# Optimization experiments

Measured on AMD Instinct MI355X. Metric: run time of the kernel, lower is better.

The kernel has to match this reference:

```python
import jax, jax.numpy as jnp
import numpy as np

TOP_K = 2  # num_experts_per_tok


def setup_inputs() -> dict:
    key = jax.random.key(0)
    ks = jax.random.split(key, 5)
    B, S, D, M, E = 4, 2048, 2048, 2048, 8
    x = jax.random.normal(ks[0], (B, S, D), dtype=jnp.float32)
    gate_kernel = jax.random.normal(ks[1], (D, E), dtype=jnp.float32) / np.sqrt(D)
    wi_0 = jax.random.normal(ks[2], (E, D, M), dtype=jnp.float32) / np.sqrt(D)
    wi_1 = jax.random.normal(ks[3], (E, D, M), dtype=jnp.float32) / np.sqrt(D)
    wo = jax.random.normal(ks[4], (E, M, D), dtype=jnp.float32) / np.sqrt(M)
    return {"x": x, "gate_kernel": gate_kernel, "wi_0": wi_0, "wi_1": wi_1, "wo": wo}


def reference(x, gate_kernel, wi_0, wi_1, wo):
    E = gate_kernel.shape[-1]
    # Gate logits: (B, S, E)
    gate_logits = jnp.einsum("bsd,de->bse", x, gate_kernel)
    # Top-k routing, then softmax over the selected experts' logits
    top_k_weights, top_k_indices = jax.lax.top_k(gate_logits, TOP_K)
    top_k_weights = jax.nn.softmax(top_k_weights.astype(jnp.float32), axis=-1).astype(x.dtype)
    # Dense combine weights per expert: (B, S, E)
    combine_w = jnp.sum(
        jax.nn.one_hot(top_k_indices, E, dtype=x.dtype) * top_k_weights[..., None], axis=-2
    )
    # Grouped GEMM (dense-masked form, as in MaxText dense_matmul path)
    h0 = jnp.einsum("bsd,edm->bsem", x, wi_0)  # (B, S, E, M)
    h1 = jnp.einsum("bsd,edm->bsem", x, wi_1)
    h = jax.nn.silu(h0) * h1 * combine_w[..., None]
    out = jnp.einsum("bsem,emd->bsd", h, wo)  # (B, S, D)
    return out
```

## Files before the change

### kernel.cpp

```cpp
#include <hip/hip_runtime.h>
#include <hip/hip_bf16.h>
#include <stdint.h>

#define TT   8192
#define DD   2048
#define MM   2048
#define NE   8

typedef float f32x4 __attribute__((ext_vector_type(4)));
typedef short s16x8 __attribute__((ext_vector_type(8)));
typedef unsigned int u32;
typedef unsigned long long u64;

static __device__ __forceinline__ short f2bf(float f) {
  __hip_bfloat16 h = __float2bfloat16(f);
  short s;
  __builtin_memcpy(&s, &h, 2);
  return s;
}
static __device__ __forceinline__ float bf2f(short s) {
  u32 u = ((u32)(unsigned short)s) << 16;
  float f;
  __builtin_memcpy(&f, &u, 4);
  return f;
}

static __device__ __forceinline__ void gload_lds16(const short* g, short* lds) {
  __builtin_amdgcn_global_load_lds(
      (const __attribute__((address_space(1))) u32*)g,
      (__attribute__((address_space(3))) u32*)lds, 16, 0, 0);
}

#define VM2()  asm volatile("s_waitcnt vmcnt(2)" ::: "memory")
#define VM0()  asm volatile("s_waitcnt vmcnt(0)" ::: "memory")
#define LG0()  asm volatile("s_waitcnt lgkmcnt(0)" ::: "memory")
#define BAR()  __builtin_amdgcn_s_barrier()

__global__ __launch_bounds__(256) void tcvt01_kernel(
    const float* __restrict__ w0, const float* __restrict__ w1,
    short* __restrict__ o0, short* __restrict__ o1) {
  __shared__ short tile[64][65];
  const int bz = blockIdx.z;
  const float* in  = (bz < 8) ? w0 : w1;
  short* out       = (bz < 8) ? o0 : o1;
  const int ex = bz & 7;
  const float* src = in + (size_t)ex * DD * MM;
  short* dst = out + (size_t)ex * DD * MM;
  const int r0 = blockIdx.y * 64;
  const int c0 = blockIdx.x * 64;
  const int t = threadIdx.x;
  const int rr = t >> 4, cc = (t & 15) * 4;
  #pragma unroll
  for (int i = 0; i < 4; i++) {
    int row = rr + i * 16;
    f32x4 v = *(const f32x4*)(src + (size_t)(r0 + row) * MM + c0 + cc);
    tile[cc + 0][row] = f2bf(v[0]);
    tile[cc + 1][row] = f2bf(v[1]);
    tile[cc + 2][row] = f2bf(v[2]);
    tile[cc + 3][row] = f2bf(v[3]);
  }
  __syncthreads();
  const int orow = t >> 2, c8 = (t & 3) * 16;
  s16x8 v0, v1;
  #pragma unroll
  for (int i = 0; i < 8; i++) { v0[i] = tile[orow][c8 + i]; v1[i] = tile[orow][c8 + 8 + i]; }
  short* dp = dst + (size_t)(c0 + orow) * DD + r0 + c8;
  *(s16x8*)(dp) = v0;
  *(s16x8*)(dp + 8) = v1;
}

__global__ __launch_bounds__(256) void gate_kernel(const float* __restrict__ x,
    const float* __restrict__ gk, int* __restrict__ counts,
    int* __restrict__ tkidx, float* __restrict__ tkw, short* __restrict__ xbf) {
  int t = blockIdx.x;
  const float* xr = x + (size_t)t * DD;
  const int d0 = threadIdx.x * 8;
  f32x4 a = *(const f32x4*)(xr + d0);
  f32x4 b = *(const f32x4*)(xr + d0 + 4);
  s16x8 v;
  v[0]=f2bf(a[0]); v[1]=f2bf(a[1]); v[2]=f2bf(a[2]); v[3]=f2bf(a[3]);
  v[4]=f2bf(b[0]); v[5]=f2bf(b[1]); v[6]=f2bf(b[2]); v[7]=f2bf(b[3]);
  *(s16x8*)(xbf + (size_t)t * DD + d0) = v;

  float acc[NE];
  #pragma unroll
  for (int e = 0; e < NE; e++) acc[e] = 0.f;
  #pragma unroll
  for (int j = 0; j < 8; j++) {
    float xv = (j < 4) ? a[j] : b[j - 4];
    const float* g = gk + (size_t)(d0 + j) * NE;
    #pragma unroll
    for (int e = 0; e < NE; e++) acc[e] += xv * g[e];
  }
  #pragma unroll
  for (int e = 0; e < NE; e++) {
    #pragma unroll
    for (int off = 32; off >= 1; off >>= 1)
      acc[e] += __shfl_xor(acc[e], off, 64);
  }
  __shared__ float red[4][NE];
  int wid = threadIdx.x >> 6;
  int lane = threadIdx.x & 63;
  if (lane == 0) {
    #pragma unroll
    for (int e = 0; e < NE; e++) red[wid][e] = acc[e];
  }
  __syncthreads();
  if (threadIdx.x == 0) {
    float l[NE];
    #pragma unroll
    for (int e = 0; e < NE; e++) l[e] = red[0][e] + red[1][e] + red[2][e] + red[3][e];
    int i1 = 0; float v1 = l[0];
    #pragma unroll
    for (int e = 1; e < NE; e++) if (l[e] > v1) { v1 = l[e]; i1 = e; }
    int i2 = -1; float v2 = -1e30f;
    #pragma unroll
    for (int e = 0; e < NE; e++) if (e != i1 && l[e] > v2) { v2 = l[e]; i2 = e; }
    float p = __expf(v2 - v1);
    float inv = 1.f / (1.f + p);
    tkidx[t*2]   = i1; tkidx[t*2+1] = i2;
    tkw[t*2]     = inv; tkw[t*2+1]  = p * inv;
    atomicAdd(&counts[i1], 1);
    atomicAdd(&counts[i2], 1);
  }
}

__global__ __launch_bounds__(256) void scatter_kernel(const int* __restrict__ counts,
    int* __restrict__ offsets, const int* __restrict__ tkidx,
    const float* __restrict__ tkw, int* __restrict__ ltok, float* __restrict__ lwt,
    int* __restrict__ slots) {
  const int e = blockIdx.x;
  const int tid = threadIdx.x;
  const int wid = tid >> 6, lane = tid & 63;
  __shared__ int base_s;
  __shared__ int wsum[4];
  if (tid == 0) {
    int s = 0;
    #pragma unroll
    for (int i = 0; i < NE; i++) {
      if (e == 0) offsets[i] = s;
      if (i < e) s += counts[i];
      else if (e == 0) s += counts[i];
    }
    if (e == 0) offsets[NE] = s;
    int bs = 0;
    for (int i = 0; i < e; i++) bs += counts[i];
    base_s = bs;
  }
  __syncthreads();
  int base = base_s;
  for (int it = 0; it < (TT * 2) / 256; it++) {
    int i = it * 256 + tid;
    bool m = (tkidx[i] == e);
    u64 b = __ballot(m);
    if (lane == 0) wsum[wid] = __popcll(b);
    __syncthreads();
    int pre = 0;
    #pragma unroll
    for (int w = 0; w < 4; w++) if (w < wid) pre += wsum[w];
    int tot = wsum[0] + wsum[1] + wsum[2] + wsum[3];
    int rank = __popcll(b & ((lane == 0) ? 0ull : ((1ull << lane) - 1ull)));
    if (m) {
      int dst = base + pre + rank;
      ltok[dst] = i >> 1;
      lwt[dst]  = tkw[i];
      slots[i]  = dst;
    }
    __syncthreads();
    base += tot;
  }
}

__global__ __launch_bounds__(256) void combine_kernel(const short* __restrict__ comb,
    const int* __restrict__ slots, float* __restrict__ out) {
  const int t = blockIdx.x;
  const int s0 = slots[2 * t], s1 = slots[2 * t + 1];
  const int idx = threadIdx.x;
  s16x8 a = *(const s16x8*)(comb + (size_t)s0 * DD + idx * 8);
  s16x8 b = *(const s16x8*)(comb + (size_t)s1 * DD + idx * 8);
  f32x4 o0, o1;
  #pragma unroll
  for (int j = 0; j < 4; j++) {
    o0[j] = bf2f(a[j]) + bf2f(b[j]);
    o1[j] = bf2f(a[4 + j]) + bf2f(b[4 + j]);
  }
  float* po = out + (size_t)t * DD + idx * 8;
  *(f32x4*)(po) = o0;
  *(f32x4*)(po + 4) = o1;
}

__device__ __forceinline__ void find_seg(const int* __restrict__ offsets, int tile, int bm,
                                         int& e, int& row0, int& rows, int& seg) {
  e = -1; row0 = 0; rows = 0; seg = 0;
  int accT = 0, prev = offsets[0];
  #pragma unroll
  for (int i = 0; i < NE; i++) {
    int nxt = offsets[i+1];
    int cnt = nxt - prev;
    int nt = (cnt + bm - 1) / bm;
    if (e < 0 && tile < accT + nt) { e = i; row0 = (tile - accT) * bm; rows = cnt; seg = prev; }
    accT += nt; prev = nxt;
  }
}

__device__ __forceinline__ void xcd_map(int ypx, int& tile, int& nyi) {
  const int bid = blockIdx.y * gridDim.x + blockIdx.x;
  const int xcd = bid & 7;
  const int i = bid >> 3;
  tile = i / ypx;
  nyi  = xcd * ypx + (i % ypx);
}

#define G1TILES 136
#define G1GRID  (G1TILES * 16)
#define GOGRID  (8 * 32 * 32)

__global__ __launch_bounds__(256, 2) void gemm1_fused(
    const short* __restrict__ xbf,
    const short* __restrict__ w0t, const short* __restrict__ w1t,
    const int* __restrict__ offsets,
    const int* __restrict__ ltok, const float* __restrict__ lwt,
    short* __restrict__ hbuf,
    const float* __restrict__ wo, short* __restrict__ wot) {
  __shared__ short As[128 * 64];
  __shared__ short B0s[128 * 64];
  __shared__ short B1s[128 * 64];
  __shared__ float w_s[128];

  const int bid = blockIdx.x;
  if (bid >= G1GRID) {
    short (*tile)[65] = (short(*)[65])As;
    const int idx = bid - G1GRID;
    const int ex = idx >> 10;
    const int rem = idx & 1023;
    const int r0 = (rem >> 5) * 64;
    const int c0 = (rem & 31) * 64;
    const float* src = wo + (size_t)ex * DD * MM;
    short* dst = wot + (size_t)ex * DD * MM;
    const int t = threadIdx.x;
    const int rr = t >> 4, cc = (t & 15) * 4;
    #pragma unroll
    for (int i = 0; i < 4; i++) {
      int row = rr + i * 16;
      f32x4 v = *(const f32x4*)(src + (size_t)(r0 + row) * MM + c0 + cc);
      tile[cc + 0][row] = f2bf(v[0]);
      tile[cc + 1][row] = f2bf(v[1]);
      tile[cc + 2][row] = f2bf(v[2]);
      tile[cc + 3][row] = f2bf(v[3]);
    }
    __syncthreads();
    const int orow = t >> 2, c8 = (t & 3) * 16;
    s16x8 v0, v1;
    #pragma unroll
    for (int i = 0; i < 8; i++) { v0[i] = tile[orow][c8 + i]; v1[i] = tile[orow][c8 + 8 + i]; }
    short* dp = dst + (size_t)(c0 + orow) * DD + r0 + c8;
    *(s16x8*)(dp) = v0;
    *(s16x8*)(dp + 8) = v1;
    return;
  }

  const int xcd = bid & 7;
  const int bi = bid >> 3;
  const int tile = bi >> 1;
  const int nyi = xcd * 2 + (bi & 1);
  const int n0 = nyi * 128;
  int e, row0, rows, seg;
  find_seg(offsets, tile, 128, e, row0, rows, seg);
  if (e < 0) return;

  const int tid = threadIdx.x;
  const int lane = tid & 63, wid = tid >> 6;
  if (tid < 128) {
    int gr = row0 + tid;
    w_s[tid] = (gr < rows) ? lwt[seg + gr] : 0.f;
  }

  const int swz = ((lane & 7) ^ (lane >> 3)) * 8;
  const short* abase[4];
  const short* b0base[4];
  const short* b1base[4];
  #pragma unroll
  for (int c = 0; c < 4; c++) {
    int chunk = wid * 4 + c;
    int r = chunk * 8 + (lane >> 3);
    int gr = row0 + r; if (gr >= rows) gr = rows - 1;
    int tok = ltok[seg + gr];
    abase[c]  = xbf + (size_t)tok * DD + swz;
    int n = n0 + r;
    b0base[c] = w0t + ((size_t)e * MM + n) * DD + swz;
    b1base[c] = w1t + ((size_t)e * MM + n) * DD + swz;
  }

  const int wr = wid >> 1, wc = wid & 1;
  const int lr = lane & 15;
  const int kq = (lane >> 4) * 8;

  f32x4 acc0[4][4], acc1[4][4];
  #pragma unroll
  for (int i = 0; i < 4; i++)
    #pragma unroll
    for (int j = 0; j < 4; j++) { acc0[i][j] = 0.f; acc1[i][j] = 0.f; }

  for (int k0 = 0; k0 < DD; k0 += 64) {
    #pragma unroll
    for (int c = 0; c < 4; c++) {
      int chunk = wid * 4 + c;
      gload_lds16(abase[c]  + k0, As  + chunk * 512);
      gload_lds16(b0base[c] + k0, B0s + chunk * 512);
      gload_lds16(b1base[c] + k0, B1s + chunk * 512);
    }
    __syncthreads();

    #pragma unroll
    for (int ks = 0; ks < 2; ks++) {
      s16x8 a[4], b0[4], b1[4];
      #pragma unroll
      for (int mi = 0; mi < 4; mi++) {
        int row = wr * 64 + mi * 16 + lr;
        int koff = (ks * 32 + kq) ^ ((row & 7) * 8);
        a[mi] = *(const s16x8*)&As[row * 64 + koff];
      }
      #pragma unroll
      for (int ni = 0; ni < 4; ni++) {
        int row = wc * 64 + ni * 16 + lr;
        int koff = (ks * 32 + kq) ^ ((row & 7) * 8);
        b0[ni] = *(const s16x8*)&B0s[row * 64 + koff];
        b1[ni] = *(const s16x8*)&B1s[row * 64 + koff];
      }
      #pragma unroll
      for (int mi = 0; mi < 4; mi++)
        #pragma unroll
        for (int ni = 0; ni < 4; ni++) {
          acc0[mi][ni] = __builtin_amdgcn_mfma_f32_16x16x32_bf16(a[mi], b0[ni], acc0[mi][ni], 0, 0, 0);
          acc1[mi][ni] = __builtin_amdgcn_mfma_f32_16x16x32_bf16(a[mi], b1[ni], acc1[mi][ni], 0, 0, 0);
        }
    }
    __syncthreads();
  }

  const int lq = lane >> 4;
  #pragma unroll
  for (int mi = 0; mi < 4; mi++) {
    #pragma unroll
    for (int jj = 0; jj < 4; jj++) {
      int r = wr * 64 + mi * 16 + lq * 4 + jj;
      int gr = row0 + r;
      if (gr < rows) {
        float wgt = w_s[r];
        size_t hrow = (size_t)(seg + gr) * MM + n0;
        #pragma unroll
        for (int ni = 0; ni < 4; ni++) {
          int c = wc * 64 + ni * 16 + lr;
          float g = acc0[mi][ni][jj];
          float u = acc1[mi][ni][jj];
          float act = g / (1.f + __expf(-g));
          hbuf[hrow + c] = f2bf(act * u * wgt);
        }
      }
    }
  }
}

#define MAXT2 72

__global__ __launch_bounds__(512, 2) void gemm2_fast(
    const short* __restrict__ hbuf,
    const short* __restrict__ wot,
    const int* __restrict__ offsets,
    short* __restrict__ comb) {
  __shared__ short As[2][256 * 64];
  __shared__ short Bs[2][256 * 64];

  int tile, nyi;
  xcd_map(1, tile, nyi);
  const int n0 = nyi * 256;
  int e, row0, rows, seg;
  find_seg(offsets, tile, 256, e, row0, rows, seg);
  if (e < 0) return;

  const int tid = threadIdx.x;
  const int lane = tid & 63, wid = tid >> 6;
  const int srow = tid >> 3;
  const int swz = ((tid & 7) ^ (srow & 7)) * 8;

  const short* aP[2][2];
  const short* bP[2][2];
  #pragma unroll
  for (int h = 0; h < 2; h++)
    #pragma unroll
    for (int rd = 0; rd < 2; rd++) {
      int gr = row0 + h * 128 + rd * 64 + srow;
      if (gr >= rows) gr = rows - 1;
      aP[h][rd] = hbuf + (size_t)(seg + gr) * MM + swz;
      int n = n0 + h * 128 + rd * 64 + srow;
      bP[h][rd] = wot + ((size_t)e * DD + n) * MM + swz;
    }
  const short* aP00 = aP[0][0]; const short* aP01 = aP[0][1];
  const short* aP10 = aP[1][0]; const short* aP11 = aP[1][1];
  const short* bP00 = bP[0][0]; const short* bP01 = bP[0][1];
  const short* bP10 = bP[1][0]; const short* bP11 = bP[1][1];

  const int wr = wid >> 2, wn = wid & 3;
  const int lr = lane & 15;
  const int kq = (lane >> 4) * 8;
  const int lq = lane >> 4;

  f32x4 acc[8][4];
  #pragma unroll
  for (int i = 0; i < 8; i++)
    #pragma unroll
    for (int j = 0; j < 4; j++) acc[i][j] = 0.f;

  int brow_[4], bkey_[4];
  #pragma unroll
  for (int ni = 0; ni < 4; ni++) {
    brow_[ni] = wn * 64 + ni * 16 + lr;
    bkey_[ni] = (brow_[ni] & 7) * 8;
  }
  int arowL_[4], akeyL_[4], arowH_[4], akeyH_[4];
  #pragma unroll
  for (int mi = 0; mi < 4; mi++) {
    arowL_[mi] = wr * 128 + mi * 16 + lr;        akeyL_[mi] = (arowL_[mi] & 7) * 8;
    arowH_[mi] = wr * 128 + (mi + 4) * 16 + lr;  akeyH_[mi] = (arowH_[mi] & 7) * 8;
  }

  const int wofs = wid * 512;
  auto stA0 = [&](int buf, int kof) {
    short* d = &As[buf][0];
    gload_lds16(aP00 + kof, d + wofs);
    gload_lds16(aP01 + kof, d + 4096 + wofs);
  };
  auto stA1 = [&](int buf, int kof) {
    short* d = &As[buf][128 * 64];
    gload_lds16(aP10 + kof, d + wofs);
    gload_lds16(aP11 + kof, d + 4096 + wofs);
  };
  auto stB0 = [&](int buf, int kof) {
    short* d = &Bs[buf][0];
    gload_lds16(bP00 + kof, d + wofs);
    gload_lds16(bP01 + kof, d + 4096 + wofs);
  };
  auto stB1 = [&](int buf, int kof) {
    short* d = &Bs[buf][128 * 64];
    gload_lds16(bP10 + kof, d + wofs);
    gload_lds16(bP11 + kof, d + 4096 + wofs);
  };

  stA0(0, 0); stB0(0, 0); stB1(0, 0); stA1(0, 0);
  stA0(1, 64);
  VM2();
  BAR();

  const int NIT = (MM / 64) / 2;
  s16x8 av[4], bv[4], bw[4];

  for (int it = 0; it < NIT; ++it) {
    const bool pf = (it + 1 < NIT);
    const int kb  = (2 * it + 1) * 64;
    const int kna = (2 * it + 2) * 64;
    const int knb = (2 * it + 3) * 64;

    #pragma unroll
    for (int mi = 0; mi < 4; mi++) av[mi] = *(const s16x8*)&As[0][arowL_[mi] * 64 + (kq ^ akeyL_[mi])];
    #pragma unroll
    for (int ni = 0; ni < 4; ni++) bv[ni] = *(const s16x8*)&Bs[0][brow_[ni] * 64 + (kq ^ bkey_[ni])];
    stB0(1, kb);
    BAR(); LG0();
    __builtin_amdgcn_s_setprio(1);
    #pragma unroll
    for (int mi = 0; mi < 4; mi++)
      #pragma unroll
      for (int ni = 0; ni < 4; ni++)
        acc[mi][ni] = __builtin_amdgcn_mfma_f32_16x16x32_bf16(av[mi], bv[ni], acc[mi][ni], 0, 0, 0);
    __builtin_amdgcn_s_setprio(0);
    BAR();

    #pragma unroll
    for (int mi = 0; mi < 4; mi++) av[mi] = *(const s16x8*)&As[0][arowH_[mi] * 64 + (kq ^ akeyH_[mi])];
    stB1(1, kb);
    BAR(); LG0();
    __builtin_amdgcn_s_setprio(1);
    #pragma unroll
    for (int mi = 0; mi < 4; mi++)
      #pragma unroll
      for (int ni = 0; ni < 4; ni++)
        acc[mi + 4][ni] = __builtin_amdgcn_mfma_f32_16x16x32_bf16(av[mi], bv[ni], acc[mi + 4][ni], 0, 0, 0);
    __builtin_amdgcn_s_setprio(0);
    BAR();

    #pragma unroll
    for (int mi = 0; mi < 4; mi++) av[mi] = *(const s16x8*)&As[0][arowL_[mi] * 64 + ((32 + kq) ^ akeyL_[mi])];
    #pragma unroll
    for (int ni = 0; ni < 4; ni++) bw[ni] = *(const s16x8*)&Bs[0][brow_[ni] * 64 + ((32 + kq) ^ bkey_[ni])];
    stA1(1, kb);
    BAR(); LG0();
    __builtin_amdgcn_s_setprio(1);
    #pragma unroll
    for (int mi = 0; mi < 4; mi++)
      #pragma unroll
      for (int ni = 0; ni < 4; ni++)
        acc[mi][ni] = __builtin_amdgcn_mfma_f32_16x16x32_bf16(av[mi], bw[ni], acc[mi][ni], 0, 0, 0);
    __builtin_amdgcn_s_setprio(0);
    BAR();

    #pragma unroll
    for (int mi = 0; mi < 4; mi++) av[mi] = *(const s16x8*)&As[0][arowH_[mi] * 64 + ((32 + kq) ^ akeyH_[mi])];
    if (pf) stA0(0, kna);
    BAR(); LG0();
    __builtin_amdgcn_s_setprio(1);
    #pragma unroll
    for (int mi = 0; mi < 4; mi++)
      #pragma unroll
      for (int ni = 0; ni < 4; ni++)
        acc[mi + 4][ni] = __builtin_amdgcn_mfma_f32_16x16x32_bf16(av[mi], bw[ni], acc[mi + 4][ni], 0, 0, 0);
    __builtin_amdgcn_s_setprio(0);
    if (pf) { VM2(); } else { VM0(); }
    BAR();

    #pragma unroll
    for (int mi = 0; mi < 4; mi++) av[mi] = *(const s16x8*)&As[1][arowL_[mi] * 64 + (kq ^ akeyL_[mi])];
    #pragma unroll
    for (int ni = 0; ni < 4; ni++) bv[ni] = *(const s16x8*)&Bs[1][brow_[ni] * 64 + (kq ^ bkey_[ni])];
    if (pf) stB0(0, kna);
    BAR(); LG0();
    __builtin_amdgcn_s_setprio(1);
    #pragma unroll
    for (int mi = 0; mi < 4; mi++)
      #pragma unroll
      for (int ni = 0; ni < 4; ni++)
        acc[mi][ni] = __builtin_amdgcn_mfma_f32_16x16x32_bf16(av[mi], bv[ni], acc[mi][ni], 0, 0, 0);
    __builtin_amdgcn_s_setprio(0);
    BAR();

    #pragma unroll
    for (int mi = 0; mi < 4; mi++) av[mi] = *(const s16x8*)&As[1][arowH_[mi] * 64 + (kq ^ akeyH_[mi])];
    if (pf) stB1(0, kna);
    BAR(); LG0();
    __builtin_amdgcn_s_setprio(1);
    #pragma unroll
    for (int mi = 0; mi < 4; mi++)
      #pragma unroll
      for (int ni = 0; ni < 4; ni++)
        acc[mi + 4][ni] = __builtin_amdgcn_mfma_f32_16x16x32_bf16(av[mi], bv[ni], acc[mi + 4][ni], 0, 0, 0);
    __builtin_amdgcn_s_setprio(0);
    BAR();

    #pragma unroll
    for (int mi = 0; mi < 4; mi++) av[mi] = *(const s16x8*)&As[1][arowL_[mi] * 64 + ((32 + kq) ^ akeyL_[mi])];
    #pragma unroll
    for (int ni = 0; ni < 4; ni++) bw[ni] = *(const s16x8*)&Bs[1][brow_[ni] * 64 + ((32 + kq) ^ bkey_[ni])];
    if (pf) stA1(0, kna);
    BAR(); LG0();
    __builtin_amdgcn_s_setprio(1);
    #pragma unroll
    for (int mi = 0; mi < 4; mi++)
      #pragma unroll
      for (int ni = 0; ni < 4; ni++)
        acc[mi][ni] = __builtin_amdgcn_mfma_f32_16x16x32_bf16(av[mi], bw[ni], acc[mi][ni], 0, 0, 0);
    __builtin_amdgcn_s_setprio(0);
    BAR();

    #pragma unroll
    for (int mi = 0; mi < 4; mi++) av[mi] = *(const s16x8*)&As[1][arowH_[mi] * 64 + ((32 + kq) ^ akeyH_[mi])];
    if (pf) stA0(1, knb);
    BAR(); LG0();
    __builtin_amdgcn_s_setprio(1);
    #pragma unroll
    for (int mi = 0; mi < 4; mi++)
      #pragma unroll
      for (int ni = 0; ni < 4; ni++)
        acc[mi + 4][ni] = __builtin_amdgcn_mfma_f32_16x16x32_bf16(av[mi], bw[ni], acc[mi + 4][ni], 0, 0, 0);
    __builtin_amdgcn_s_setprio(0);
    if (pf) { VM2(); BAR(); }
  }

  #pragma unroll
  for (int mi = 0; mi < 8; mi++) {
    #pragma unroll
    for (int jj = 0; jj < 4; jj++) {
      int r = wr * 128 + mi * 16 + lq * 4 + jj;
      int gr = row0 + r;
      if (gr < rows) {
        size_t orow = (size_t)(seg + gr) * DD + n0;
        #pragma unroll
        for (int ni = 0; ni < 4; ni++) {
          int c = wn * 64 + ni * 16 + lr;
          comb[orow + c] = f2bf(acc[mi][ni][jj]);
        }
      }
    }
  }
}

extern "C" void kernel_launch(void* const* d_in, const int* in_sizes, int n_in,
                              void* d_out, int out_size, void* d_ws, size_t ws_size,
                              hipStream_t stream) {
  const float* x   = (const float*)d_in[0];
  const float* gk  = (const float*)d_in[1];
  const float* wi0 = (const float*)d_in[2];
  const float* wi1 = (const float*)d_in[3];
  const float* wo  = (const float*)d_in[4];
  float* out = (float*)d_out;

  char* w = (char*)d_ws;
  int*   counts  = (int*)(w);
  int*   offsets = (int*)(w + 256);
  int*   tkidx   = (int*)(w + 1024);
  float* tkw     = (float*)(w + 1024 + 65536);
  int*   ltok    = (int*)(w + 1024 + 2*65536);
  float* lwt     = (float*)(w + 1024 + 3*65536);
  int*   slots   = (int*)(w + 1024 + 4*65536);
  short* xbf  = (short*)(w + 524288);
  short* hbuf = xbf + (size_t)TT * DD;
  short* w0t  = hbuf + (size_t)2 * TT * MM;
  short* w1t  = w0t + (size_t)NE * DD * MM;
  short* wot  = w1t + (size_t)NE * DD * MM;
  short* comb = w0t;

  hipMemsetAsync(counts, 0, 64, stream);

  gate_kernel<<<TT, 256, 0, stream>>>(x, gk, counts, tkidx, tkw, xbf);
  scatter_kernel<<<NE, 256, 0, stream>>>(counts, offsets, tkidx, tkw, ltok, lwt, slots);
  tcvt01_kernel<<<dim3(MM/64, DD/64, 16), 256, 0, stream>>>(wi0, wi1, w0t, w1t);

  gemm1_fused<<<G1GRID + GOGRID, 256, 0, stream>>>(xbf, w0t, w1t, offsets, ltok, lwt,
                                                   hbuf, wo, wot);
  gemm2_fast<<<dim3(MAXT2, DD/256), 512, 0, stream>>>(hbuf, wot, offsets, comb);
  combine_kernel<<<TT, 256, 0, stream>>>(comb, slots, out);
}
```

Before: 855.0 us.

## Fuse expert combine into GEMM2 epilogue via atomics and merge gate with weight conversion

The second GEMM's epilogue now writes each routed row straight into the fp32 output at its token's row, using atomicAdd through a per-tile token index table held in LDS. This removes the bf16 intermediate buffer, the slot map and the separate combine kernel. In exchange the output must be zeroed with a memset, and the epilogue issues many global float atomics. Separately, the gate/top-k kernel and the wi0/wi1 transpose-convert kernel are merged into one launch with a larger grid, which saves a launch and lets the two overlap.

```diff
diff --git a/kernel.cpp b/kernel.cpp
--- a/kernel.cpp
+++ b/kernel.cpp
@@ -18,12 +18,6 @@
   __builtin_memcpy(&s, &h, 2);
   return s;
 }
-static __device__ __forceinline__ float bf2f(short s) {
-  u32 u = ((u32)(unsigned short)s) << 16;
-  float f;
-  __builtin_memcpy(&f, &u, 4);
-  return f;
-}
 
 static __device__ __forceinline__ void gload_lds16(const short* g, short* lds) {
   __builtin_amdgcn_global_load_lds(
@@ -36,43 +30,52 @@
 #define LG0()  asm volatile("s_waitcnt lgkmcnt(0)" ::: "memory")
 #define BAR()  __builtin_amdgcn_s_barrier()
 
-__global__ __launch_bounds__(256) void tcvt01_kernel(
-    const float* __restrict__ w0, const float* __restrict__ w1,
+#define GCVT01  (16 * 32 * 32)
+
+__global__ __launch_bounds__(256) void gate_fused(
+    const float* __restrict__ x, const float* __restrict__ gk,
+    int* __restrict__ counts, int* __restrict__ tkidx, float* __restrict__ tkw,
+    short* __restrict__ xbf,
+    const float* __restrict__ wi0, const float* __restrict__ wi1,
     short* __restrict__ o0, short* __restrict__ o1) {
   __shared__ short tile[64][65];
-  const int bz = blockIdx.z;
-  const float* in  = (bz < 8) ? w0 : w1;
-  short* out       = (bz < 8) ? o0 : o1;
-  const int ex = bz & 7;
-  const float* src = in + (size_t)ex * DD * MM;
-  short* dst = out + (size_t)ex * DD * MM;
-  const int r0 = blockIdx.y * 64;
-  const int c0 = blockIdx.x * 64;
-  const int t = threadIdx.x;
-  const int rr = t >> 4, cc = (t & 15) * 4;
-  #pragma unroll
-  for (int i = 0; i < 4; i++) {
-    int row = rr + i * 16;
-    f32x4 v = *(const f32x4*)(src + (size_t)(r0 + row) * MM + c0 + cc);
-    tile[cc + 0][row] = f2bf(v[0]);
-    tile[cc + 1][row] = f2bf(v[1]);
-    tile[cc + 2][row] = f2bf(v[2]);
-    tile[cc + 3][row] = f2bf(v[3]);
-  }
-  __syncthreads();
-  const int orow = t >> 2, c8 = (t & 3) * 16;
-  s16x8 v0, v1;
-  #pragma unroll
-  for (int i = 0; i < 8; i++) { v0[i] = tile[orow][c8 + i]; v1[i] = tile[orow][c8 + 8 + i]; }
-  short* dp = dst + (size_t)(c0 + orow) * DD + r0 + c8;
-  *(s16x8*)(dp) = v0;
-  *(s16x8*)(dp + 8) = v1;
-}
-
-__global__ __launch_bounds__(256) void gate_kernel(const float* __restrict__ x,
-    const float* __restrict__ gk, int* __restrict__ counts,
-    int* __restrict__ tkidx, float* __restrict__ tkw, short* __restrict__ xbf) {
-  int t = blockIdx.x;
+  __shared__ float red[4][NE];
+
+  const int bid = blockIdx.x;
+  if (bid >= TT) {
+    const int idx = bid - TT;
+    const int wz = idx >> 10;
+    const float* in  = (wz < 8) ? wi0 : wi1;
+    short* out       = (wz < 8) ? o0 : o1;
+    const int ex = wz & 7;
+    const int rem = idx & 1023;
+    const int r0 = (rem >> 5) * 64;
+    const int c0 = (rem & 31) * 64;
+    const float* src = in + (size_t)ex * DD * MM;
+    short* dst = out + (size_t)ex * DD * MM;
+    const int t = threadIdx.x;
+    const int rr = t >> 4, cc = (t & 15) * 4;
+    #pragma unroll
+    for (int i = 0; i < 4; i++) {
+      int row = rr + i * 16;
+      f32x4 v = *(const f32x4*)(src + (size_t)(r0 + row) * MM + c0 + cc);
+      tile[cc + 0][row] = f2bf(v[0]);
+      tile[cc + 1][row] = f2bf(v[1]);
+      tile[cc + 2][row] = f2bf(v[2]);
+      tile[cc + 3][row] = f2bf(v[3]);
+    }
+    __syncthreads();
+    const int orow = t >> 2, c8 = (t & 3) * 16;
+    s16x8 v0, v1;
+    #pragma unroll
+    for (int i = 0; i < 8; i++) { v0[i] = tile[orow][c8 + i]; v1[i] = tile[orow][c8 + 8 + i]; }
+    short* dp = dst + (size_t)(c0 + orow) * DD + r0 + c8;
+    *(s16x8*)(dp) = v0;
+    *(s16x8*)(dp + 8) = v1;
+    return;
+  }
+
+  const int t = bid;
   const float* xr = x + (size_t)t * DD;
   const int d0 = threadIdx.x * 8;
   f32x4 a = *(const f32x4*)(xr + d0);
@@ -98,7 +101,6 @@
     for (int off = 32; off >= 1; off >>= 1)
       acc[e] += __shfl_xor(acc[e], off, 64);
   }
-  __shared__ float red[4][NE];
   int wid = threadIdx.x >> 6;
   int lane = threadIdx.x & 63;
   if (lane == 0) {
@@ -127,8 +129,7 @@
 
 __global__ __launch_bounds__(256) void scatter_kernel(const int* __restrict__ counts,
     int* __restrict__ offsets, const int* __restrict__ tkidx,
-    const float* __restrict__ tkw, int* __restrict__ ltok, float* __restrict__ lwt,
-    int* __restrict__ slots) {
+    const float* __restrict__ tkw, int* __restrict__ ltok, float* __restrict__ lwt) {
   const int e = blockIdx.x;
   const int tid = threadIdx.x;
   const int wid = tid >> 6, lane = tid & 63;
@@ -164,29 +165,10 @@
       int dst = base + pre + rank;
       ltok[dst] = i >> 1;
       lwt[dst]  = tkw[i];
-      slots[i]  = dst;
     }
     __syncthreads();
     base += tot;
   }
-}
-
-__global__ __launch_bounds__(256) void combine_kernel(const short* __restrict__ comb,
-    const int* __restrict__ slots, float* __restrict__ out) {
-  const int t = blockIdx.x;
-  const int s0 = slots[2 * t], s1 = slots[2 * t + 1];
-  const int idx = threadIdx.x;
-  s16x8 a = *(const s16x8*)(comb + (size_t)s0 * DD + idx * 8);
-  s16x8 b = *(const s16x8*)(comb + (size_t)s1 * DD + idx * 8);
-  f32x4 o0, o1;
-  #pragma unroll
-  for (int j = 0; j < 4; j++) {
-    o0[j] = bf2f(a[j]) + bf2f(b[j]);
-    o1[j] = bf2f(a[4 + j]) + bf2f(b[4 + j]);
-  }
-  float* po = out + (size_t)t * DD + idx * 8;
-  *(f32x4*)(po) = o0;
-  *(f32x4*)(po + 4) = o1;
 }
 
 __device__ __forceinline__ void find_seg(const int* __restrict__ offsets, int tile, int bm,
@@ -367,9 +349,11 @@
     const short* __restrict__ hbuf,
     const short* __restrict__ wot,
     const int* __restrict__ offsets,
-    short* __restrict__ comb) {
+    const int* __restrict__ ltok,
+    float* __restrict__ out) {
   __shared__ short As[2][256 * 64];
   __shared__ short Bs[2][256 * 64];
+  __shared__ int tok_s[256];
 
   int tile, nyi;
   xcd_map(1, tile, nyi);
@@ -380,6 +364,10 @@
 
   const int tid = threadIdx.x;
   const int lane = tid & 63, wid = tid >> 6;
+  if (tid < 256) {
+    int gr = row0 + tid;
+    tok_s[tid] = (gr < rows) ? ltok[seg + gr] : -1;
+  }
   const int srow = tid >> 3;
   const int swz = ((tid & 7) ^ (srow & 7)) * 8;
 
@@ -581,11 +569,11 @@
       int r = wr * 128 + mi * 16 + lq * 4 + jj;
       int gr = row0 + r;
       if (gr < rows) {
-        size_t orow = (size_t)(seg + gr) * DD + n0;
+        size_t orow = (size_t)tok_s[r] * DD + n0;
         #pragma unroll
         for (int ni = 0; ni < 4; ni++) {
           int c = wn * 64 + ni * 16 + lr;
-          comb[orow + c] = f2bf(acc[mi][ni][jj]);
+          atomicAdd(&out[orow + c], acc[mi][ni][jj]);
         }
       }
     }
@@ -609,22 +597,20 @@
   float* tkw     = (float*)(w + 1024 + 65536);
   int*   ltok    = (int*)(w + 1024 + 2*65536);
   float* lwt     = (float*)(w + 1024 + 3*65536);
-  int*   slots   = (int*)(w + 1024 + 4*65536);
   short* xbf  = (short*)(w + 524288);
   short* hbuf = xbf + (size_t)TT * DD;
   short* w0t  = hbuf + (size_t)2 * TT * MM;
   short* w1t  = w0t + (size_t)NE * DD * MM;
   short* wot  = w1t + (size_t)NE * DD * MM;
-  short* comb = w0t;
 
   hipMemsetAsync(counts, 0, 64, stream);
-
-  gate_kernel<<<TT, 256, 0, stream>>>(x, gk, counts, tkidx, tkw, xbf);
-  scatter_kernel<<<NE, 256, 0, stream>>>(counts, offsets, tkidx, tkw, ltok, lwt, slots);
-  tcvt01_kernel<<<dim3(MM/64, DD/64, 16), 256, 0, stream>>>(wi0, wi1, w0t, w1t);
+  hipMemsetAsync(out, 0, sizeof(float) * (size_t)out_size, stream);
+
+  gate_fused<<<TT + GCVT01, 256, 0, stream>>>(x, gk, counts, tkidx, tkw, xbf,
+                                              wi0, wi1, w0t, w1t);
+  scatter_kernel<<<NE, 256, 0, stream>>>(counts, offsets, tkidx, tkw, ltok, lwt);
 
   gemm1_fused<<<G1GRID + GOGRID, 256, 0, stream>>>(xbf, w0t, w1t, offsets, ltok, lwt,
                                                    hbuf, wo, wot);
-  gemm2_fast<<<dim3(MAXT2, DD/256), 512, 0, stream>>>(hbuf, wot, offsets, comb);
-  combine_kernel<<<TT, 256, 0, stream>>>(comb, slots, out);
-}
+  gemm2_fast<<<dim3(MAXT2, DD/256), 512, 0, stream>>>(hbuf, wot, offsets, ltok, out);
+}
```

Result: slower. 899.1 us (+5.1%).
